# Optimization experiments

Measured on AMD Instinct MI355X. Metric: run time of the kernel, lower is better.

## Reference

```python
import jax, jax.numpy as jnp
import numpy as np

B, T, D, H = 4, 1024, 512, 8
DK = D // H
L = 2 * T - 1  # relative-position length, Transformer-XL convention


def setup_inputs() -> dict:
    key = jax.random.key(0)
    ks = jax.random.split(key, 16)
    s = 0.02  # xavier-ish init scale
    inp = {
        "query": jax.random.normal(ks[0], (B, T, D), jnp.float32),
        "key": jax.random.normal(ks[1], (B, T, D), jnp.float32),
        "value": jax.random.normal(ks[2], (B, T, D), jnp.float32),
        "pos_embedding": jax.random.normal(ks[3], (B, L, D), jnp.float32),
        "mask": jax.random.randint(ks[4], (B, T), 0, 2).astype(bool),
        # nn.Linear weights are [out, in]; y = x @ W.T + b
        "Wq": jax.random.normal(ks[5], (D, D), jnp.float32) * s,
        "bq": jnp.zeros((D,), jnp.float32),
        "Wk": jax.random.normal(ks[6], (D, D), jnp.float32) * s,
        "bk": jnp.zeros((D,), jnp.float32),
        "Wv": jax.random.normal(ks[7], (D, D), jnp.float32) * s,
        "bv": jnp.zeros((D,), jnp.float32),
        "Wr": jax.random.normal(ks[8], (D, D), jnp.float32) * s,  # rpe_proj, no bias
        "u_bias": jax.random.normal(ks[9], (H, DK), jnp.float32) * s,
        "v_bias": jax.random.normal(ks[10], (H, DK), jnp.float32) * s,
        "Wo": jax.random.normal(ks[11], (D, D), jnp.float32) * s,
        "bo": jnp.zeros((D,), jnp.float32),
    }
    return inp


def _rel_shift(x):
    # x: [B, H, T, L] -> Transformer-XL pad/reshape/slice shift, keep first L//2+1 cols
    b, h, t, l = x.shape
    x = jnp.pad(x, ((0, 0), (0, 0), (0, 0), (1, 0)))        # [B,H,T,L+1]
    x = x.reshape(b, h, l + 1, t)[:, :, 1:, :]               # drop first row
    x = x.reshape(b, h, t, l)
    return x[..., : l // 2 + 1]                              # [B,H,T,T]


def reference(query, key, value, pos_embedding, mask,
              Wq, bq, Wk, bk, Wv, bv, Wr, u_bias, v_bias, Wo, bo):
    b = query.shape[0]
    q = (query @ Wq.T + bq).reshape(b, -1, H, DK)            # [B,T,H,dk]
    k = (key @ Wk.T + bk).reshape(b, -1, H, DK)              # [B,T,H,dk]
    v = (value @ Wv.T + bv).reshape(b, -1, H, DK)            # [B,T,H,dk]
    r = (pos_embedding @ Wr.T).reshape(b, -1, H, DK)         # [B,L,H,dk]

    main = jnp.einsum('bthd,bshd->bhts', q + u_bias, k)      # content score
    rpe = jnp.einsum('bthd,blhd->bhtl', q + v_bias, r)       # [B,H,T,L]

    scores = (main + _rel_shift(rpe)) / np.sqrt(DK).astype(np.float32)
    scores = jnp.where(mask[:, None, None, :],
                       jnp.asarray(1e-4, scores.dtype), scores)
    attn = jax.nn.softmax(scores, axis=-1)                   # dropout off (eval)

    out = jnp.einsum('bhts,bshd->bhtd', attn, v)             # [B,H,T,dk]
    # Faithful to original: view(B,-1,d_model) WITHOUT transposing heads back
    out = out.reshape(b, -1, D)                              # [B,T,D] (head-interleaved)
    return out @ Wo.T + bo
```

## Files before the change

kernel.cpp:

```cpp
#include <hip/hip_runtime.h>
#include <stdint.h>
#include <stddef.h>

#define B_ 4
#define T_ 1024
#define D_ 512
#define H_ 8
#define DK_ 64
#define L_ 2047
#define LP_ 2048

typedef __attribute__((ext_vector_type(8))) short short8;
typedef __attribute__((ext_vector_type(4))) short short4_t;
typedef __attribute__((ext_vector_type(4))) float f32x4;
typedef __attribute__((ext_vector_type(4))) unsigned int u32x4;
typedef __attribute__((ext_vector_type(8))) __bf16 bf16x8;

static __device__ __forceinline__ short f2bf(float f) {
  union { float f; unsigned u; } x; x.f = f;
  unsigned r = x.u + 0x7fffu + ((x.u >> 16) & 1u);
  return (short)(r >> 16);
}

static __device__ __forceinline__ f32x4 mfma16(bf16x8 a, bf16x8 b, f32x4 c) {
  return __builtin_amdgcn_mfma_f32_16x16x32_bf16(a, b, c, 0, 0, 0);
}

static __device__ __forceinline__ bf16x8 ldbf8(const short* p) {
  return *(const bf16x8*)p;
}

__global__ __launch_bounds__(256) void convert_kernel(
    const float* __restrict__ qin, const float* __restrict__ kin, const float* __restrict__ vin,
    const float* __restrict__ pin,
    const float* __restrict__ Wq, const float* __restrict__ Wk, const float* __restrict__ Wv,
    const float* __restrict__ Wr, const float* __restrict__ Wo,
    const unsigned char* __restrict__ mraw,
    short* __restrict__ dst, float* __restrict__ mask_f)
{
  if (blockIdx.x == 11518) {
    __shared__ int fmis, fany;
    if (threadIdx.x == 0) { fmis = 0; fany = 0; }
    __syncthreads();
    int lm = 0, la = 0;
    for (int i = threadIdx.x; i < B_ * T_; i += 256) {
      unsigned char c = mraw[i];
      if (c) { la = 1; if (i & 3) lm = 1; }
    }
    if (lm) atomicOr(&fmis, 1);
    if (la) atomicOr(&fany, 1);
    __syncthreads();
    int mmode = fmis ? 0 : (fany ? 1 : 2);
    const int* mi = (const int*)mraw;
    for (int i = threadIdx.x; i < B_ * T_; i += 256) {
      int mv = (mmode == 0) ? (int)mraw[i] : (mmode == 1 ? mi[i] : 0);
      mask_f[i] = mv ? 1.0f : 0.0f;
    }
    return;
  }
  int gid = blockIdx.x * 256 + threadIdx.x;
  const float* src; int base;
  if      (gid < 524288)  { src = qin; base = 0; }
  else if (gid < 1048576) { src = kin; base = 524288; }
  else if (gid < 1572864) { src = vin; base = 1048576; }
  else if (gid < 2620928) { src = pin; base = 1572864; }
  else if (gid < 2686464) { src = Wq;  base = 2620928; }
  else if (gid < 2752000) { src = Wk;  base = 2686464; }
  else if (gid < 2817536) { src = Wv;  base = 2752000; }
  else if (gid < 2883072) { src = Wr;  base = 2817536; }
  else                    { src = Wo;  base = 2883072; }
  f32x4 val = ((const f32x4*)src)[gid - base];
  short4_t o;
  o[0] = f2bf(val[0]); o[1] = f2bf(val[1]); o[2] = f2bf(val[2]); o[3] = f2bf(val[3]);
  ((short4_t*)dst)[gid] = o;
}

template<int VARIANT>
__global__ __launch_bounds__(256, 4) void proj_gemm(
    const short* __restrict__ qkv_bf, const short* __restrict__ pos_bf,
    const short* __restrict__ W_bf, const short* __restrict__ ao_bf,
    short* __restrict__ quO, short* __restrict__ qvO, short* __restrict__ khO,
    short* __restrict__ vtO, short* __restrict__ rhO, float* __restrict__ outF,
    const float* __restrict__ bq, const float* __restrict__ bk_,
    const float* __restrict__ bv_, const float* __restrict__ bo_,
    const float* __restrict__ ub, const float* __restrict__ vb)
{
  const int bid0 = blockIdx.x;
  constexpr int PER = (VARIANT == 0) ? 80 : 16;
  const int bid = (bid0 & 7) * PER + (bid0 >> 3);

  const short* A; const short* W;
  int Mtotal, mode, m0, n0;
  if constexpr (VARIANT == 0) {
    if (bid < 384) {
      int zz = bid >> 7, r2 = bid & 127;
      m0 = (r2 >> 2) * 128; n0 = (r2 & 3) * 128;
      A = qkv_bf + (size_t)zz * 2097152; W = W_bf + (size_t)zz * 262144;
      Mtotal = 4096; mode = zz;
    } else {
      int r2 = bid - 384;
      m0 = (r2 >> 2) * 128; n0 = (r2 & 3) * 128;
      A = pos_bf; W = W_bf + 786432;
      Mtotal = 8188; mode = 3;
    }
  } else {
    m0 = (bid >> 2) * 128; n0 = (bid & 3) * 128;
    A = ao_bf; W = W_bf + 1048576;
    Mtotal = 4096; mode = 4;
  }
  __shared__ __align__(16) short As[128 * 64];
  __shared__ __align__(16) short Bs[128 * 64];
  const int tid = threadIdx.x;
  const int lane = tid & 63, wid = tid >> 6;
  const int wr = wid >> 1, wc = wid & 1;
  const int l15 = lane & 15, l4 = lane >> 4;
  const int trow = tid >> 3;
  const int tcolsw = (((tid & 7) ^ (trow & 7)) << 3);

  auto STAGE = [&](int kt) {
#pragma unroll
    for (int j = 0; j < 4; j++) {
      int srow = m0 + j * 32 + trow; if (srow > Mtotal - 1) srow = Mtotal - 1;
      __builtin_amdgcn_global_load_lds(
          (const __attribute__((address_space(1))) unsigned int*)(A + (size_t)srow * 512 + kt + tcolsw),
          (__attribute__((address_space(3))) unsigned int*)(&As[(j * 32 + wid * 8) * 64]), 16, 0, 0);
    }
#pragma unroll
    for (int j = 0; j < 4; j++) {
      __builtin_amdgcn_global_load_lds(
          (const __attribute__((address_space(1))) unsigned int*)(W + (size_t)(n0 + j * 32 + trow) * 512 + kt + tcolsw),
          (__attribute__((address_space(3))) unsigned int*)(&Bs[(j * 32 + wid * 8) * 64]), 16, 0, 0);
    }
  };

  f32x4 acc[4][4] = {};

#pragma unroll
  for (int it = 0; it < 8; ++it) {
    STAGE(it * 64);
    __syncthreads();
    __builtin_amdgcn_s_setprio(1);
#pragma unroll
    for (int kf = 0; kf < 2; kf++) {
      const int colA = ((kf * 4 + l4) ^ (l15 & 7)) << 3;
      bf16x8 af[4], bf4[4];
#pragma unroll
      for (int rf = 0; rf < 4; rf++)
        af[rf] = ldbf8(&As[(wr * 64 + rf * 16 + l15) * 64 + colA]);
#pragma unroll
      for (int cf = 0; cf < 4; cf++)
        bf4[cf] = ldbf8(&Bs[(wc * 64 + cf * 16 + l15) * 64 + colA]);
#pragma unroll
      for (int rf = 0; rf < 4; rf++)
#pragma unroll
        for (int cf = 0; cf < 4; cf++)
          acc[rf][cf] = mfma16(af[rf], bf4[cf], acc[rf][cf]);
    }
    __builtin_amdgcn_s_setprio(0);
    __syncthreads();
  }

#pragma unroll
  for (int cf = 0; cf < 4; cf++) {
    int n = n0 + wc * 64 + cf * 16 + l15;
    float bias = 0.f, ubv = 0.f, vbv = 0.f;
    if (mode == 0) { bias = bq[n]; ubv = ub[n]; vbv = vb[n]; }
    else if (mode == 1) bias = bk_[n];
    else if (mode == 2) bias = bv_[n];
    else if (mode == 4) bias = bo_[n];
    int hh = n >> 6, dk = n & 63;
#pragma unroll
    for (int rf = 0; rf < 4; rf++) {
#pragma unroll
      for (int reg = 0; reg < 4; reg++) {
        int m = m0 + wr * 64 + rf * 16 + l4 * 4 + reg;
        float val = acc[rf][cf][reg] + bias;
        if (mode == 0) {
          int bb = m >> 10, t = m & 1023;
          size_t ad = ((size_t)(bb * H_ + hh) * T_ + t) * DK_ + dk;
          quO[ad] = f2bf(val + ubv);
          qvO[ad] = f2bf(val + vbv);
        } else if (mode == 1) {
          int bb = m >> 10, t = m & 1023;
          khO[((size_t)(bb * H_ + hh) * T_ + t) * DK_ + dk] = f2bf(val);
        } else if (mode == 2) {
          int bb = m >> 10, t = m & 1023;
          vtO[((size_t)(bb * H_ + hh) * DK_ + dk) * T_ + t] = f2bf(val);
        } else if (mode == 3) {
          if (m < B_ * L_) {
            int bb = m / L_;
            int ll = m - bb * L_;
            rhO[((size_t)(bb * H_ + hh) * LP_ + ll) * DK_ + dk] = f2bf(val);
          }
        } else {
          outF[(size_t)m * D_ + n] = val;
        }
      }
    }
  }
}

__global__ __launch_bounds__(256) void attn_kernel(
    const short* __restrict__ qu, const short* __restrict__ qv,
    const short* __restrict__ kh, const short* __restrict__ vt,
    const short* __restrict__ rh, const float* __restrict__ mask_f,
    short* __restrict__ attnout)
{
  const int tid = threadIdx.x;
  const int lane = tid & 63;
  const int w = tid >> 6;
  const int l15 = lane & 15, l4 = lane >> 4;
  const int bid = blockIdx.x;
  const int xcd = bid & 7, slot = bid >> 3;
  const int bh = (slot >> 4) * 8 + xcd;
  const int b = bh >> 3;
  const int t0b = (slot & 15) * 64;
  const int t0w = t0b + w * 16;
  const int woff = 48 - w * 16;

  __shared__ __align__(16) short Ks[2][64 * 64];
  __shared__ __align__(16) short Vs[2][64 * 64];
  __shared__ __align__(16) short Rs[2][128 * 64];
  __shared__ __align__(16) short Ps[4][16 * 64];

  const short* kB = kh + (size_t)bh * T_ * DK_;
  const short* vB = vt + (size_t)bh * DK_ * T_;
  const short* rB = rh + (size_t)bh * LP_ * DK_;

  const short* quB = qu + ((size_t)bh * T_ + t0w + l15) * DK_ + l4 * 8;
  const short* qvB = qv + ((size_t)bh * T_ + t0w + l15) * DK_ + l4 * 8;
  bf16x8 quf0 = ldbf8(quB), quf1 = ldbf8(quB + 32);
  bf16x8 qvf0 = ldbf8(qvB), qvf1 = ldbf8(qvB + 32);

  const short8 ones_s = {(short)0x3F80, (short)0x3F80, (short)0x3F80, (short)0x3F80,
                         (short)0x3F80, (short)0x3F80, (short)0x3F80, (short)0x3F80};
  const bf16x8 ones8 = __builtin_bit_cast(bf16x8, ones_s);

  const int trow = tid >> 3;
  const int tcol = (((tid & 7) ^ ((tid >> 3) & 7)) << 3);
  const int wbase = w * 512;

  auto STAGE = [&](int buf, int s0) {
    const int l0b = 960 + s0 - t0b;
#pragma unroll
    for (int j = 0; j < 2; j++) {
      __builtin_amdgcn_global_load_lds(
          (const __attribute__((address_space(1))) unsigned int*)(kB + (size_t)(s0 + trow + j * 32) * 64 + tcol),
          (__attribute__((address_space(3))) unsigned int*)(&Ks[buf][j * 2048 + wbase]), 16, 0, 0);
      __builtin_amdgcn_global_load_lds(
          (const __attribute__((address_space(1))) unsigned int*)(vB + (size_t)(trow + j * 32) * T_ + s0 + tcol),
          (__attribute__((address_space(3))) unsigned int*)(&Vs[buf][j * 2048 + wbase]), 16, 0, 0);
    }
#pragma unroll
    for (int j = 0; j < 4; j++) {
      __builtin_amdgcn_global_load_lds(
          (const __attribute__((address_space(1))) unsigned int*)(rB + (size_t)(l0b + trow + j * 32) * 64 + tcol),
          (__attribute__((address_space(3))) unsigned int*)(&Rs[buf][j * 2048 + wbase]), 16, 0, 0);
    }
  };

  float* Msf = (float*)&Ps[0][0];
  ((f32x4*)Msf)[tid] = ((const f32x4*)(mask_f + b * T_))[tid];
  STAGE(0, 0);
  __syncthreads();
  unsigned long long mbits = 0ull;
#pragma unroll
  for (int it = 0; it < 16; ++it)
#pragma unroll
    for (int cf = 0; cf < 4; ++cf)
      if (Msf[it * 64 + cf * 16 + l15] != 0.f)
        mbits |= 1ull << (it * 4 + cf);
  __syncthreads();

  f32x4 accO[4] = {};
  f32x4 sum_acc = {};

  const int swz = (l15 & 7) << 3;

  for (int it = 0; it < 16; ++it) {
    const int s0 = it << 6;
    const int cur = it & 1;
    if (it < 15) STAGE(cur ^ 1, s0 + 64);

    const unsigned m4 = (unsigned)(mbits >> (it * 4)) & 15u;

    f32x4 sacc[4] = {};
    f32x4 gacc[5] = {};
    __builtin_amdgcn_s_setprio(1);
#pragma unroll
    for (int kf = 0; kf < 2; kf++) {
      const int col = (kf * 32 + l4 * 8) ^ swz;
      bf16x8 qf = kf ? quf1 : quf0;
      bf16x8 vf_ = kf ? qvf1 : qvf0;
#pragma unroll
      for (int cf = 0; cf < 4; cf++)
        sacc[cf] = mfma16(qf, ldbf8(&Ks[cur][(cf * 16 + l15) * 64 + col]), sacc[cf]);
#pragma unroll
      for (int gf = 0; gf < 5; gf++)
        gacc[gf] = mfma16(vf_, ldbf8(&Rs[cur][(woff + gf * 16 + l15) * 64 + col]), gacc[gf]);
    }
    __builtin_amdgcn_s_setprio(0);

    float p[4][4];
#pragma unroll
    for (int r = 0; r < 4; r++) {
      const int tl = l4 * 4 + r;
      const int e = l15 + 15 - tl;
      const int src = (lane & 48) | (e & 15);
      float sh0 = __shfl(gacc[0][r], src);
      float sh1 = __shfl(gacc[1][r], src);
      float sh2 = __shfl(gacc[2][r], src);
      float sh3 = __shfl(gacc[3][r], src);
      float sh4 = __shfl(gacc[4][r], src);
      float ga[4] = {sh0, sh1, sh2, sh3};
      float gb[4] = {sh1, sh2, sh3, sh4};
#pragma unroll
      for (int cf = 0; cf < 4; cf++) {
        float gg = (e < 16) ? ga[cf] : gb[cf];
        float lg = (sacc[cf][r] + gg) * 0.125f;
        lg = (m4 & (1u << cf)) ? 1e-4f : lg;
        p[r][cf] = __expf(lg);
      }
    }

#pragma unroll
    for (int r = 0; r < 4; r++) {
      const int tl = l4 * 4 + r;
      const int sw2 = (tl & 7) << 3;
#pragma unroll
      for (int cf = 0; cf < 4; cf++)
        Ps[w][tl * 64 + ((cf * 16 + l15) ^ sw2)] = f2bf(p[r][cf]);
    }

    __builtin_amdgcn_s_setprio(1);
#pragma unroll
    for (int kf = 0; kf < 2; kf++) {
      const int kc = kf * 32 + l4 * 8;
      bf16x8 pa = ldbf8(&Ps[w][l15 * 64 + (kc ^ swz)]);
      sum_acc = mfma16(pa, ones8, sum_acc);
#pragma unroll
      for (int vf = 0; vf < 4; vf++)
        accO[vf] = mfma16(pa, ldbf8(&Vs[cur][(vf * 16 + l15) * 64 + (kc ^ swz)]), accO[vf]);
    }
    __builtin_amdgcn_s_setprio(0);
    __syncthreads();
  }

#pragma unroll
  for (int r = 0; r < 4; r++) {
    const int tl = l4 * 4 + r;
    float inv = 1.0f / sum_acc[r];
#pragma unroll
    for (int vf = 0; vf < 4; vf++) {
      float val = accO[vf][r] * inv;
      attnout[((size_t)bh * T_ + t0w + tl) * DK_ + vf * 16 + l15] = f2bf(val);
    }
  }
}

extern "C" void kernel_launch(void* const* d_in, const int* in_sizes, int n_in,
                              void* d_out, int out_size, void* d_ws, size_t ws_size,
                              hipStream_t stream) {
  const float* qin = (const float*)d_in[0];
  const float* kin = (const float*)d_in[1];
  const float* vin = (const float*)d_in[2];
  const float* pin = (const float*)d_in[3];
  const unsigned char* mraw = (const unsigned char*)d_in[4];
  const float* Wq = (const float*)d_in[5];
  const float* bq = (const float*)d_in[6];
  const float* Wk = (const float*)d_in[7];
  const float* bk = (const float*)d_in[8];
  const float* Wv = (const float*)d_in[9];
  const float* bv = (const float*)d_in[10];
  const float* Wr = (const float*)d_in[11];
  const float* ub = (const float*)d_in[12];
  const float* vb = (const float*)d_in[13];
  const float* Wo = (const float*)d_in[14];
  const float* bo = (const float*)d_in[15];
  float* out = (float*)d_out;
  char* ws = (char*)d_ws;

  short* qkv_bf = (short*)(ws + 0);
  short* pos_bf = (short*)(ws + 12582912);
  short* W_bf   = (short*)(ws + 20967424);
  float* mask_f = (float*)(ws + 23588864);
  short* quW    = (short*)(ws + 23605248);
  short* qvW    = (short*)(ws + 27799552);
  short* khW    = (short*)(ws + 31993856);
  short* vtW    = (short*)(ws + 36188160);
  short* rhW    = (short*)(ws + 40382464);
  short* aoW    = (short*)(ws + 48771072);

  convert_kernel<<<dim3(11519), dim3(256), 0, stream>>>(
      qin, kin, vin, pin, Wq, Wk, Wv, Wr, Wo, mraw, qkv_bf, mask_f);
  proj_gemm<0><<<dim3(640), dim3(256), 0, stream>>>(
      qkv_bf, pos_bf, W_bf, aoW, quW, qvW, khW, vtW, rhW, nullptr,
      bq, bk, bv, bo, ub, vb);
  attn_kernel<<<dim3(512), dim3(256), 0, stream>>>(
      quW, qvW, khW, vtW, rhW, mask_f, aoW);
  proj_gemm<1><<<dim3(128), dim3(256), 0, stream>>>(
      qkv_bf, pos_bf, W_bf, aoW, quW, qvW, khW, vtW, rhW, out,
      bq, bk, bv, bo, ub, vb);
}
```

Before: 104.1 us.

## Load relative-position fragments directly from global memory instead of staging through LDS

Removes the shared-memory double buffer for the relative-position tile and has each lane load its R fragments straight from global memory into registers, interleaving those loads with the K-score MFMAs. This halves the LDS footprint per block, and the launch bound now requests four blocks per CU to use the freed space for occupancy. The cost is redundant global and L2 traffic, since waves no longer share one staged R tile, plus extra register pressure under the tighter occupancy bound.

```diff
diff --git a/kernel.cpp b/kernel.cpp
--- a/kernel.cpp
+++ b/kernel.cpp
@@ -200,7 +200,7 @@
   }
 }
 
-__global__ __launch_bounds__(256) void attn_kernel(
+__global__ __launch_bounds__(256, 4) void attn_kernel(
     const short* __restrict__ qu, const short* __restrict__ qv,
     const short* __restrict__ kh, const short* __restrict__ vt,
     const short* __restrict__ rh, const float* __restrict__ mask_f,
@@ -216,11 +216,9 @@
   const int b = bh >> 3;
   const int t0b = (slot & 15) * 64;
   const int t0w = t0b + w * 16;
-  const int woff = 48 - w * 16;
 
   __shared__ __align__(16) short Ks[2][64 * 64];
   __shared__ __align__(16) short Vs[2][64 * 64];
-  __shared__ __align__(16) short Rs[2][128 * 64];
   __shared__ __align__(16) short Ps[4][16 * 64];
 
   const short* kB = kh + (size_t)bh * T_ * DK_;
@@ -232,6 +230,8 @@
   bf16x8 quf0 = ldbf8(quB), quf1 = ldbf8(quB + 32);
   bf16x8 qvf0 = ldbf8(qvB), qvf1 = ldbf8(qvB + 32);
 
+  const short* rLane = rB + (size_t)(1008 - t0w + l15) * 64 + l4 * 8;
+
   const short8 ones_s = {(short)0x3F80, (short)0x3F80, (short)0x3F80, (short)0x3F80,
                          (short)0x3F80, (short)0x3F80, (short)0x3F80, (short)0x3F80};
   const bf16x8 ones8 = __builtin_bit_cast(bf16x8, ones_s);
@@ -241,7 +241,6 @@
   const int wbase = w * 512;
 
   auto STAGE = [&](int buf, int s0) {
-    const int l0b = 960 + s0 - t0b;
 #pragma unroll
     for (int j = 0; j < 2; j++) {
       __builtin_amdgcn_global_load_lds(
@@ -251,12 +250,6 @@
           (const __attribute__((address_space(1))) unsigned int*)(vB + (size_t)(trow + j * 32) * T_ + s0 + tcol),
           (__attribute__((address_space(3))) unsigned int*)(&Vs[buf][j * 2048 + wbase]), 16, 0, 0);
     }
-#pragma unroll
-    for (int j = 0; j < 4; j++) {
-      __builtin_amdgcn_global_load_lds(
-          (const __attribute__((address_space(1))) unsigned int*)(rB + (size_t)(l0b + trow + j * 32) * 64 + tcol),
-          (__attribute__((address_space(3))) unsigned int*)(&Rs[buf][j * 2048 + wbase]), 16, 0, 0);
-    }
   };
 
   float* Msf = (float*)&Ps[0][0];
@@ -280,6 +273,12 @@
   for (int it = 0; it < 16; ++it) {
     const int s0 = it << 6;
     const int cur = it & 1;
+    const short* rIt = rLane + (size_t)s0 * 64;
+
+    bf16x8 r0[5];
+#pragma unroll
+    for (int gf = 0; gf < 5; gf++) r0[gf] = ldbf8(rIt + gf * 1024);
+
     if (it < 15) STAGE(cur ^ 1, s0 + 64);
 
     const unsigned m4 = (unsigned)(mbits >> (it * 4)) & 15u;
@@ -287,18 +286,27 @@
     f32x4 sacc[4] = {};
     f32x4 gacc[5] = {};
     __builtin_amdgcn_s_setprio(1);
-#pragma unroll
-    for (int kf = 0; kf < 2; kf++) {
-      const int col = (kf * 32 + l4 * 8) ^ swz;
-      bf16x8 qf = kf ? quf1 : quf0;
-      bf16x8 vf_ = kf ? qvf1 : qvf0;
+    {
+      const int col0 = (l4 * 8) ^ swz;
 #pragma unroll
       for (int cf = 0; cf < 4; cf++)
-        sacc[cf] = mfma16(qf, ldbf8(&Ks[cur][(cf * 16 + l15) * 64 + col]), sacc[cf]);
-#pragma unroll
-      for (int gf = 0; gf < 5; gf++)
-        gacc[gf] = mfma16(vf_, ldbf8(&Rs[cur][(woff + gf * 16 + l15) * 64 + col]), gacc[gf]);
-    }
+        sacc[cf] = mfma16(quf0, ldbf8(&Ks[cur][(cf * 16 + l15) * 64 + col0]), sacc[cf]);
+    }
+    bf16x8 r1[5];
+#pragma unroll
+    for (int gf = 0; gf < 5; gf++) r1[gf] = ldbf8(rIt + gf * 1024 + 32);
+#pragma unroll
+    for (int gf = 0; gf < 5; gf++)
+      gacc[gf] = mfma16(qvf0, r0[gf], gacc[gf]);
+    {
+      const int col1 = (32 + l4 * 8) ^ swz;
+#pragma unroll
+      for (int cf = 0; cf < 4; cf++)
+        sacc[cf] = mfma16(quf1, ldbf8(&Ks[cur][(cf * 16 + l15) * 64 + col1]), sacc[cf]);
+    }
+#pragma unroll
+    for (int gf = 0; gf < 5; gf++)
+      gacc[gf] = mfma16(qvf1, r1[gf], gacc[gf]);
     __builtin_amdgcn_s_setprio(0);
 
     float p[4][4];
```

New measurement: 126.9 us. 1.22x slower.

## Split attention key range across two blocks and add combine kernel

Applied to the files above, without the earlier changes.

Attention blocks now each process half of the key sequence, which doubles the grid to 1024 blocks. Each block writes unnormalized fp32 partial outputs and row sums, and a new combine kernel adds the two halves and normalizes them. The u/v biases are now applied inside the attention kernel, so the projection writes a single q tensor instead of two. LDS double buffering is dropped in favour of single buffers with launch_bounds(256,4) for higher occupancy. The cost is an extra kernel launch, fp32 partial traffic through global memory, and loads that are no longer overlapped with compute.

```diff
diff --git a/kernel.cpp b/kernel.cpp
--- a/kernel.cpp
+++ b/kernel.cpp
@@ -20,6 +20,11 @@
   union { float f; unsigned u; } x; x.f = f;
   unsigned r = x.u + 0x7fffu + ((x.u >> 16) & 1u);
   return (short)(r >> 16);
+}
+
+static __device__ __forceinline__ float bf2f(short s) {
+  union { unsigned u; float f; } x; x.u = ((unsigned)(unsigned short)s) << 16;
+  return x.f;
 }
 
 static __device__ __forceinline__ f32x4 mfma16(bf16x8 a, bf16x8 b, f32x4 c) {
@@ -79,11 +84,10 @@
 __global__ __launch_bounds__(256, 4) void proj_gemm(
     const short* __restrict__ qkv_bf, const short* __restrict__ pos_bf,
     const short* __restrict__ W_bf, const short* __restrict__ ao_bf,
-    short* __restrict__ quO, short* __restrict__ qvO, short* __restrict__ khO,
+    short* __restrict__ qO, short* __restrict__ khO,
     short* __restrict__ vtO, short* __restrict__ rhO, float* __restrict__ outF,
     const float* __restrict__ bq, const float* __restrict__ bk_,
-    const float* __restrict__ bv_, const float* __restrict__ bo_,
-    const float* __restrict__ ub, const float* __restrict__ vb)
+    const float* __restrict__ bv_, const float* __restrict__ bo_)
 {
   const int bid0 = blockIdx.x;
   constexpr int PER = (VARIANT == 0) ? 80 : 16;
@@ -163,8 +167,8 @@
 #pragma unroll
   for (int cf = 0; cf < 4; cf++) {
     int n = n0 + wc * 64 + cf * 16 + l15;
-    float bias = 0.f, ubv = 0.f, vbv = 0.f;
-    if (mode == 0) { bias = bq[n]; ubv = ub[n]; vbv = vb[n]; }
+    float bias = 0.f;
+    if (mode == 0) bias = bq[n];
     else if (mode == 1) bias = bk_[n];
     else if (mode == 2) bias = bv_[n];
     else if (mode == 4) bias = bo_[n];
@@ -177,9 +181,7 @@
         float val = acc[rf][cf][reg] + bias;
         if (mode == 0) {
           int bb = m >> 10, t = m & 1023;
-          size_t ad = ((size_t)(bb * H_ + hh) * T_ + t) * DK_ + dk;
-          quO[ad] = f2bf(val + ubv);
-          qvO[ad] = f2bf(val + vbv);
+          qO[((size_t)(bb * H_ + hh) * T_ + t) * DK_ + dk] = f2bf(val);
         } else if (mode == 1) {
           int bb = m >> 10, t = m & 1023;
           khO[((size_t)(bb * H_ + hh) * T_ + t) * DK_ + dk] = f2bf(val);
@@ -200,11 +202,12 @@
   }
 }
 
-__global__ __launch_bounds__(256) void attn_kernel(
-    const short* __restrict__ qu, const short* __restrict__ qv,
-    const short* __restrict__ kh, const short* __restrict__ vt,
-    const short* __restrict__ rh, const float* __restrict__ mask_f,
-    short* __restrict__ attnout)
+__global__ __launch_bounds__(256, 4) void attn_kernel(
+    const short* __restrict__ q, const short* __restrict__ kh,
+    const short* __restrict__ vt, const short* __restrict__ rh,
+    const float* __restrict__ mask_f,
+    const float* __restrict__ ub, const float* __restrict__ vb,
+    float* __restrict__ paccO, float* __restrict__ psum)
 {
   const int tid = threadIdx.x;
   const int lane = tid & 63;
@@ -212,25 +215,46 @@
   const int l15 = lane & 15, l4 = lane >> 4;
   const int bid = blockIdx.x;
   const int xcd = bid & 7, slot = bid >> 3;
-  const int bh = (slot >> 4) * 8 + xcd;
-  const int b = bh >> 3;
+  const int bh = (slot >> 5) * 8 + xcd;
+  const int half = (slot >> 4) & 1;
   const int t0b = (slot & 15) * 64;
+  const int b = bh >> 3, h = bh & 7;
   const int t0w = t0b + w * 16;
   const int woff = 48 - w * 16;
 
-  __shared__ __align__(16) short Ks[2][64 * 64];
-  __shared__ __align__(16) short Vs[2][64 * 64];
-  __shared__ __align__(16) short Rs[2][128 * 64];
+  __shared__ __align__(16) short Ks[64 * 64];
+  __shared__ __align__(16) short Vs[64 * 64];
+  __shared__ __align__(16) short Rs[128 * 64];
   __shared__ __align__(16) short Ps[4][16 * 64];
 
   const short* kB = kh + (size_t)bh * T_ * DK_;
   const short* vB = vt + (size_t)bh * DK_ * T_;
   const short* rB = rh + (size_t)bh * LP_ * DK_;
 
-  const short* quB = qu + ((size_t)bh * T_ + t0w + l15) * DK_ + l4 * 8;
-  const short* qvB = qv + ((size_t)bh * T_ + t0w + l15) * DK_ + l4 * 8;
-  bf16x8 quf0 = ldbf8(quB), quf1 = ldbf8(quB + 32);
-  bf16x8 qvf0 = ldbf8(qvB), qvf1 = ldbf8(qvB + 32);
+  const short* qB = q + ((size_t)bh * T_ + t0w + l15) * DK_ + l4 * 8;
+  short8 q0 = *(const short8*)qB, q1 = *(const short8*)(qB + 32);
+  const float* ubp = ub + h * 64 + l4 * 8;
+  const float* vbp = vb + h * 64 + l4 * 8;
+  f32x4 u0a = *(const f32x4*)ubp,        u0b = *(const f32x4*)(ubp + 4);
+  f32x4 u1a = *(const f32x4*)(ubp + 32), u1b = *(const f32x4*)(ubp + 36);
+  f32x4 v0a = *(const f32x4*)vbp,        v0b = *(const f32x4*)(vbp + 4);
+  f32x4 v1a = *(const f32x4*)(vbp + 32), v1b = *(const f32x4*)(vbp + 36);
+  short8 qu0s, qu1s, qv0s, qv1s;
+#pragma unroll
+  for (int j = 0; j < 4; j++) {
+    qu0s[j]     = f2bf(bf2f(q0[j])     + u0a[j]);
+    qu0s[j + 4] = f2bf(bf2f(q0[j + 4]) + u0b[j]);
+    qu1s[j]     = f2bf(bf2f(q1[j])     + u1a[j]);
+    qu1s[j + 4] = f2bf(bf2f(q1[j + 4]) + u1b[j]);
+    qv0s[j]     = f2bf(bf2f(q0[j])     + v0a[j]);
+    qv0s[j + 4] = f2bf(bf2f(q0[j + 4]) + v0b[j]);
+    qv1s[j]     = f2bf(bf2f(q1[j])     + v1a[j]);
+    qv1s[j + 4] = f2bf(bf2f(q1[j + 4]) + v1b[j]);
+  }
+  bf16x8 quf0 = __builtin_bit_cast(bf16x8, qu0s);
+  bf16x8 quf1 = __builtin_bit_cast(bf16x8, qu1s);
+  bf16x8 qvf0 = __builtin_bit_cast(bf16x8, qv0s);
+  bf16x8 qvf1 = __builtin_bit_cast(bf16x8, qv1s);
 
   const short8 ones_s = {(short)0x3F80, (short)0x3F80, (short)0x3F80, (short)0x3F80,
                          (short)0x3F80, (short)0x3F80, (short)0x3F80, (short)0x3F80};
@@ -240,49 +264,48 @@
   const int tcol = (((tid & 7) ^ ((tid >> 3) & 7)) << 3);
   const int wbase = w * 512;
 
-  auto STAGE = [&](int buf, int s0) {
+  auto STAGE = [&](int s0) {
     const int l0b = 960 + s0 - t0b;
 #pragma unroll
     for (int j = 0; j < 2; j++) {
       __builtin_amdgcn_global_load_lds(
           (const __attribute__((address_space(1))) unsigned int*)(kB + (size_t)(s0 + trow + j * 32) * 64 + tcol),
-          (__attribute__((address_space(3))) unsigned int*)(&Ks[buf][j * 2048 + wbase]), 16, 0, 0);
+          (__attribute__((address_space(3))) unsigned int*)(&Ks[j * 2048 + wbase]), 16, 0, 0);
       __builtin_amdgcn_global_load_lds(
           (const __attribute__((address_space(1))) unsigned int*)(vB + (size_t)(trow + j * 32) * T_ + s0 + tcol),
-          (__attribute__((address_space(3))) unsigned int*)(&Vs[buf][j * 2048 + wbase]), 16, 0, 0);
+          (__attribute__((address_space(3))) unsigned int*)(&Vs[j * 2048 + wbase]), 16, 0, 0);
     }
 #pragma unroll
     for (int j = 0; j < 4; j++) {
       __builtin_amdgcn_global_load_lds(
           (const __attribute__((address_space(1))) unsigned int*)(rB + (size_t)(l0b + trow + j * 32) * 64 + tcol),
-          (__attribute__((address_space(3))) unsigned int*)(&Rs[buf][j * 2048 + wbase]), 16, 0, 0);
+          (__attribute__((address_space(3))) unsigned int*)(&Rs[j * 2048 + wbase]), 16, 0, 0);
     }
   };
 
   float* Msf = (float*)&Ps[0][0];
   ((f32x4*)Msf)[tid] = ((const f32x4*)(mask_f + b * T_))[tid];
-  STAGE(0, 0);
   __syncthreads();
   unsigned long long mbits = 0ull;
 #pragma unroll
-  for (int it = 0; it < 16; ++it)
+  for (int gi = 0; gi < 16; ++gi)
 #pragma unroll
     for (int cf = 0; cf < 4; ++cf)
-      if (Msf[it * 64 + cf * 16 + l15] != 0.f)
-        mbits |= 1ull << (it * 4 + cf);
-  __syncthreads();
+      if (Msf[gi * 64 + cf * 16 + l15] != 0.f)
+        mbits |= 1ull << (gi * 4 + cf);
 
   f32x4 accO[4] = {};
   f32x4 sum_acc = {};
-
   const int swz = (l15 & 7) << 3;
-
-  for (int it = 0; it < 16; ++it) {
-    const int s0 = it << 6;
-    const int cur = it & 1;
-    if (it < 15) STAGE(cur ^ 1, s0 + 64);
-
-    const unsigned m4 = (unsigned)(mbits >> (it * 4)) & 15u;
+  const int s0base = half * 512;
+
+  for (int it = 0; it < 8; ++it) {
+    const int git = half * 8 + it;
+    const int s0 = s0base + (it << 6);
+    STAGE(s0);
+    __syncthreads();
+
+    const unsigned m4 = (unsigned)(mbits >> (git * 4)) & 15u;
 
     f32x4 sacc[4] = {};
     f32x4 gacc[5] = {};
@@ -294,10 +317,10 @@
       bf16x8 vf_ = kf ? qvf1 : qvf0;
 #pragma unroll
       for (int cf = 0; cf < 4; cf++)
-        sacc[cf] = mfma16(qf, ldbf8(&Ks[cur][(cf * 16 + l15) * 64 + col]), sacc[cf]);
+        sacc[cf] = mfma16(qf, ldbf8(&Ks[(cf * 16 + l15) * 64 + col]), sacc[cf]);
 #pragma unroll
       for (int gf = 0; gf < 5; gf++)
-        gacc[gf] = mfma16(vf_, ldbf8(&Rs[cur][(woff + gf * 16 + l15) * 64 + col]), gacc[gf]);
+        gacc[gf] = mfma16(vf_, ldbf8(&Rs[(woff + gf * 16 + l15) * 64 + col]), gacc[gf]);
     }
     __builtin_amdgcn_s_setprio(0);
 
@@ -340,7 +363,7 @@
       sum_acc = mfma16(pa, ones8, sum_acc);
 #pragma unroll
       for (int vf = 0; vf < 4; vf++)
-        accO[vf] = mfma16(pa, ldbf8(&Vs[cur][(vf * 16 + l15) * 64 + (kc ^ swz)]), accO[vf]);
+        accO[vf] = mfma16(pa, ldbf8(&Vs[(vf * 16 + l15) * 64 + (kc ^ swz)]), accO[vf]);
     }
     __builtin_amdgcn_s_setprio(0);
     __syncthreads();
@@ -349,13 +372,33 @@
 #pragma unroll
   for (int r = 0; r < 4; r++) {
     const int tl = l4 * 4 + r;
-    float inv = 1.0f / sum_acc[r];
-#pragma unroll
-    for (int vf = 0; vf < 4; vf++) {
-      float val = accO[vf][r] * inv;
-      attnout[((size_t)bh * T_ + t0w + tl) * DK_ + vf * 16 + l15] = f2bf(val);
-    }
-  }
+    const int row = bh * T_ + t0w + tl;
+#pragma unroll
+    for (int vf = 0; vf < 4; vf++)
+      paccO[(size_t)half * 2097152 + (size_t)row * 64 + vf * 16 + l15] = accO[vf][r];
+    if (l15 == 0) psum[half * 32768 + row] = sum_acc[r];
+  }
+}
+
+__global__ __launch_bounds__(256) void combine_kernel(
+    const float* __restrict__ paccO, const float* __restrict__ psum,
+    short* __restrict__ aoW)
+{
+  const int gid = blockIdx.x * 256 + threadIdx.x;
+  const int row = gid >> 3;
+  const int j8 = (gid & 7) * 8;
+  const float* a0 = paccO + (size_t)row * 64 + j8;
+  const float* a1 = a0 + 2097152;
+  f32x4 x0 = *(const f32x4*)a0,       x1 = *(const f32x4*)(a0 + 4);
+  f32x4 y0 = *(const f32x4*)a1,       y1 = *(const f32x4*)(a1 + 4);
+  const float inv = 1.0f / (psum[row] + psum[32768 + row]);
+  short8 o;
+#pragma unroll
+  for (int j = 0; j < 4; j++) {
+    o[j]     = f2bf((x0[j] + y0[j]) * inv);
+    o[j + 4] = f2bf((x1[j] + y1[j]) * inv);
+  }
+  *(short8*)(aoW + (size_t)row * 64 + j8) = o;
 }
 
 extern "C" void kernel_launch(void* const* d_in, const int* in_sizes, int n_in,
@@ -382,10 +425,11 @@
 
   short* qkv_bf = (short*)(ws + 0);
   short* pos_bf = (short*)(ws + 12582912);
+  float* paccO  = (float*)(ws + 0);
+  float* psum   = (float*)(ws + 16777216);
   short* W_bf   = (short*)(ws + 20967424);
   float* mask_f = (float*)(ws + 23588864);
-  short* quW    = (short*)(ws + 23605248);
-  short* qvW    = (short*)(ws + 27799552);
+  short* qW     = (short*)(ws + 23605248);
   short* khW    = (short*)(ws + 31993856);
   short* vtW    = (short*)(ws + 36188160);
   short* rhW    = (short*)(ws + 40382464);
@@ -394,11 +438,12 @@
   convert_kernel<<<dim3(11519), dim3(256), 0, stream>>>(
       qin, kin, vin, pin, Wq, Wk, Wv, Wr, Wo, mraw, qkv_bf, mask_f);
   proj_gemm<0><<<dim3(640), dim3(256), 0, stream>>>(
-      qkv_bf, pos_bf, W_bf, aoW, quW, qvW, khW, vtW, rhW, nullptr,
-      bq, bk, bv, bo, ub, vb);
-  attn_kernel<<<dim3(512), dim3(256), 0, stream>>>(
-      quW, qvW, khW, vtW, rhW, mask_f, aoW);
+      qkv_bf, pos_bf, W_bf, aoW, qW, khW, vtW, rhW, nullptr,
+      bq, bk, bv, bo);
+  attn_kernel<<<dim3(1024), dim3(256), 0, stream>>>(
+      qW, khW, vtW, rhW, mask_f, ub, vb, paccO, psum);
+  combine_kernel<<<dim3(1024), dim3(256), 0, stream>>>(paccO, psum, aoW);
   proj_gemm<1><<<dim3(128), dim3(256), 0, stream>>>(
-      qkv_bf, pos_bf, W_bf, aoW, quW, qvW, khW, vtW, rhW, out,
-      bq, bk, bv, bo, ub, vb);
-}
+      qkv_bf, pos_bf, W_bf, aoW, qW, khW, vtW, rhW, out,
+      bq, bk, bv, bo);
+}
```

Result: slower. 108.3 us (+4.0%).
